# Optimization experiments

Measured on AMD Instinct MI355X. Metric: run time of the kernel, lower is better.

## Reference

```python
import jax, jax.numpy as jnp
import numpy as np

B, D, F, FH = 8, 16, 16, 128
L = D * D
EPS = 1e-5


def _coords():
    i = np.arange(L, dtype=np.float64)
    c0 = ((i + 1) / D - D / 2) / (D / 2)
    c1 = ((i + 1) % D - D / 2) / (D / 2)
    return jnp.asarray(np.stack([c0, c1], axis=1), dtype=jnp.float32)  # (L, 2)


def setup_inputs() -> dict:
    key = jax.random.key(0)
    ks = jax.random.split(key, 16)
    s = 0.05
    fin = F + 2
    inp = {
        "x": jax.random.normal(ks[0], (B, F, D, D), jnp.float32),
        # g_fc1 weight split into the x_i half (first f+2 cols) and x_j half
        "W1a": jax.random.normal(ks[1], (fin, FH), jnp.float32) * s,
        "W1b": jax.random.normal(ks[2], (fin, FH), jnp.float32) * s,
        "b1": jnp.zeros((FH,), jnp.float32),
        "g1_gamma": jnp.ones((FH,), jnp.float32), "g1_beta": jnp.zeros((FH,), jnp.float32),
        "W2": jax.random.normal(ks[3], (FH, FH), jnp.float32) * s, "b2": jnp.zeros((FH,), jnp.float32),
        "g2_gamma": jnp.ones((FH,), jnp.float32), "g2_beta": jnp.zeros((FH,), jnp.float32),
        "W3": jax.random.normal(ks[4], (FH, FH), jnp.float32) * s, "b3": jnp.zeros((FH,), jnp.float32),
        "g3_gamma": jnp.ones((FH,), jnp.float32), "g3_beta": jnp.zeros((FH,), jnp.float32),
        "Wagg": jax.random.normal(ks[5], (L,), jnp.float32) * s, "bagg": jnp.zeros((), jnp.float32),
        "Wf": jax.random.normal(ks[6], (FH, FH), jnp.float32) * s, "bf": jnp.zeros((FH,), jnp.float32),
        "f_gamma": jnp.ones((FH,), jnp.float32), "f_beta": jnp.zeros((FH,), jnp.float32),
        "Wo2": jax.random.normal(ks[7], (FH, FH), jnp.float32) * s, "bo2": jnp.zeros((FH,), jnp.float32),
        "o2_gamma": jnp.ones((FH,), jnp.float32), "o2_beta": jnp.zeros((FH,), jnp.float32),
        "Wo3": jax.random.normal(ks[8], (FH, F), jnp.float32) * s, "bo3": jnp.zeros((F,), jnp.float32),
        "coord": _coords(),
    }
    return inp


def _bn(h, gamma, beta):
    # torch BatchNorm1d (training mode) applied over channel dim = last axis here;
    # stats over (batch, length), biased variance.
    mu = jnp.mean(h, axis=(0, 1))
    var = jnp.mean((h - mu) ** 2, axis=(0, 1))
    return gamma * (h - mu) * jax.lax.rsqrt(var + EPS) + beta


def reference(x, W1a, W1b, b1, g1_gamma, g1_beta, W2, b2, g2_gamma, g2_beta,
              W3, b3, g3_gamma, g3_beta, Wagg, bagg, Wf, bf, f_gamma, f_beta,
              Wo2, bo2, o2_gamma, o2_beta, Wo3, bo3, coord):
    b, f, d = x.shape[0], x.shape[1], x.shape[2]
    l = d * d
    x_flat = x.reshape(b, f, l).transpose(0, 2, 1)                     # (b, L, f)
    x_flat = jnp.concatenate([x_flat, jnp.broadcast_to(coord, (b, l, 2))], axis=2)  # (b, L, f+2)
    # g_fc1 on cat([x_i, x_j]): x_i varies along pair-dim2 (index l), x_j along dim1 (index k)
    hi = x_flat @ W1a                                                  # (b, L, FH)
    hj = x_flat @ W1b                                                  # (b, L, FH)
    h = hi[:, None, :, :] + hj[:, :, None, :] + b1                     # (b, L, L, FH)
    h = h.reshape(b, l * l, -1)
    h = jax.nn.relu(_bn(h, g1_gamma, g1_beta))
    h = jax.nn.relu(_bn(h @ W2 + b2, g2_gamma, g2_beta))
    h = jax.nn.relu(_bn(h @ W3 + b3, g3_gamma, g3_beta))
    x_g = h.reshape(b, l, l, -1)                                       # (b, k, l, FH)
    # affine_aggregate: Linear(L -> 1) over the l (dim2) axis after permute
    x_agg = jnp.einsum('bklf,l->bkf', x_g, Wagg) + bagg                # (b, L, FH)
    x_f = jax.nn.relu(_bn(x_agg @ Wf + bf, f_gamma, f_beta))
    xo = jax.nn.relu(_bn(x_f @ Wo2 + bo2, o2_gamma, o2_beta))
    out = xo @ Wo3 + bo3                                               # (b, L, f)
    return out.reshape(b, d, d, f).transpose(0, 3, 1, 2)               # (b, f, d, d)
```

## Files before the change

### kernel.cpp

```cpp
#include <hip/hip_runtime.h>
#include <hip/hip_bf16.h>

typedef __bf16 bf16x8 __attribute__((ext_vector_type(8)));
typedef float  f32x4  __attribute__((ext_vector_type(4)));

static constexpr size_t HI_OFF  = 0;
static constexpr size_t HJ_OFF  = HI_OFF + (1u << 20);
static constexpr size_t Z_OFF   = HJ_OFF + (1u << 20);
static constexpr size_t PS_OFF  = Z_OFF + (size_t)524288 * 128 * 2;
static constexpr size_t PQ_OFF  = PS_OFF + (size_t)4096 * 128 * 4;
static constexpr size_t S1I_OFF = PQ_OFF + (size_t)4096 * 128 * 4;
static constexpr size_t S2I_OFF = S1I_OFF + 4096;
static constexpr size_t S1J_OFF = S2I_OFF + 4096;
static constexpr size_t S2J_OFF = S1J_OFF + 4096;
static constexpr size_t A1_OFF  = S2J_OFF + 4096;
static constexpr size_t D1_OFF  = A1_OFF + 512;
static constexpr size_t A2_OFF  = D1_OFF + 512;
static constexpr size_t C2_OFF  = A2_OFF + 512;
static constexpr size_t A3_OFF  = C2_OFF + 512;
static constexpr size_t C3_OFF  = A3_OFF + 512;
static constexpr size_t AF_OFF  = C3_OFF + 512;
static constexpr size_t CF_OFF  = AF_OFF + 512;
static constexpr size_t AO_OFF  = CF_OFF + 512;
static constexpr size_t CO_OFF  = AO_OFF + 512;
static constexpr size_t W2T_OFF = CO_OFF + 512;
static constexpr size_t W3T_OFF = W2T_OFF + 32768;
static constexpr size_t XAGG_OFF = W3T_OFF + 32768;
static constexpr size_t Y1_OFF  = XAGG_OFF + (1u << 20);
static constexpr size_t Y2_OFF  = Y1_OFF + (1u << 20);
static constexpr size_t TPS_OFF = Y2_OFF + (1u << 20);
static constexpr size_t TPQ_OFF = TPS_OFF + 65536;

__global__ void build_h(const float* __restrict__ x, const float* __restrict__ coord,
                        const float* __restrict__ W1a, const float* __restrict__ W1b,
                        float* __restrict__ hi, float* __restrict__ hj)
{
    __shared__ float xr[18];
    int bl = blockIdx.x;
    int b = bl >> 8, l = bl & 255;
    int t = threadIdx.x;
    if (t < 18)
        xr[t] = (t < 16) ? x[((size_t)b * 16 + t) * 256 + l] : coord[l * 2 + (t - 16)];
    __syncthreads();
    float ai = 0.f, aj = 0.f;
#pragma unroll
    for (int c = 0; c < 18; ++c) {
        float xv = xr[c];
        ai += xv * W1a[c * 128 + t];
        aj += xv * W1b[c * 128 + t];
    }
    hi[(size_t)bl * 128 + t] = ai;
    hj[(size_t)bl * 128 + t] = aj;
}

__global__ void stats1(const float* __restrict__ hi, const float* __restrict__ hj,
                       float* __restrict__ S1i, float* __restrict__ S2i,
                       float* __restrict__ S1j, float* __restrict__ S2j)
{
    int b = blockIdx.x, f = threadIdx.x;
    float s1i = 0, s2i = 0, s1j = 0, s2j = 0;
    for (int l = 0; l < 256; ++l) {
        float vi = hi[((size_t)b * 256 + l) * 128 + f];
        float vj = hj[((size_t)b * 256 + l) * 128 + f];
        s1i += vi; s2i += vi * vi;
        s1j += vj; s2j += vj * vj;
    }
    S1i[b * 128 + f] = s1i; S2i[b * 128 + f] = s2i;
    S1j[b * 128 + f] = s1j; S2j[b * 128 + f] = s2j;
}

__global__ void bn1_finalize(const float* __restrict__ S1i, const float* __restrict__ S2i,
                             const float* __restrict__ S1j, const float* __restrict__ S2j,
                             const float* __restrict__ g, const float* __restrict__ be,
                             float* __restrict__ a1, float* __restrict__ d1,
                             const float* __restrict__ W2, const float* __restrict__ W3,
                             __bf16* __restrict__ W2t, __bf16* __restrict__ W3t)
{
    int f = threadIdx.x;
    float s1i = 0, s2i = 0, s1j = 0, s2j = 0;
    float mib[8], mjb[8];
#pragma unroll
    for (int b = 0; b < 8; ++b) {
        float x1 = S1i[b * 128 + f]; s1i += x1; mib[b] = x1 * (1.f / 256.f);
        s2i += S2i[b * 128 + f];
        float x2 = S1j[b * 128 + f]; s1j += x2; mjb[b] = x2 * (1.f / 256.f);
        s2j += S2j[b * 128 + f];
    }
    const float invN = 1.f / 2048.f;
    float mi = s1i * invN, mj = s1j * invN;
    float vu = s2i * invN - mi * mi;
    float vv = s2j * invN - mj * mj;
    float cr = 0.f;
#pragma unroll
    for (int b = 0; b < 8; ++b) cr += (mib[b] - mi) * (mjb[b] - mj);
    cr *= (1.f / 8.f);
    float var = vu + vv + 2.f * cr;
    float av = g[f] * rsqrtf(var + 1e-5f);
    a1[f] = av;
    d1[f] = be[f] - av * (mi + mj);
    for (int k = 0; k < 128; ++k) {
        W2t[f * 128 + k] = (__bf16)W2[k * 128 + f];
        W3t[f * 128 + k] = (__bf16)W3[k * 128 + f];
    }
}

__global__ __launch_bounds__(256) void pair_gemm1(
    const float* __restrict__ hi, const float* __restrict__ hj,
    const float* __restrict__ a1, const float* __restrict__ d1,
    const __bf16* __restrict__ W2t,
    __bf16* __restrict__ Z, float* __restrict__ ps, float* __restrict__ pq)
{
    __shared__ __align__(16) char hA[32768];
    __shared__ __align__(16) char wB[32768];
    __shared__ float red[1024];

    int blk = blockIdx.x;
    int half = blk & 1;
    int bk = blk >> 1;
    int b = bk >> 8;
    int t = threadIdx.x;
    int lane = t & 63;
    int wave = t >> 6;
    int fc = (t & 15) * 8;
    int rg = t >> 4;

    float a1v[8], qv[8];
    const float* hjrow = hj + (size_t)bk * 128 + fc;
    const float* d1p = d1 + fc;
    const float* a1p = a1 + fc;
#pragma unroll
    for (int j = 0; j < 8; ++j) { a1v[j] = a1p[j]; qv[j] = a1v[j] * hjrow[j] + d1p[j]; }

    const float* hib = hi + ((size_t)b * 256 + half * 128) * 128;
#pragma unroll
    for (int rr = 0; rr < 128; rr += 16) {
        int row = rr + rg;
        const float* src = hib + row * 128 + fc;
        bf16x8 v;
#pragma unroll
        for (int j = 0; j < 8; ++j) {
            float h = fmaxf(a1v[j] * src[j] + qv[j], 0.f);
            v[j] = (__bf16)h;
        }
        int byte = (row * 256 + fc * 2) ^ ((row & 7) << 4);
        *reinterpret_cast<bf16x8*>(hA + byte) = v;
        bf16x8 w = *reinterpret_cast<const bf16x8*>(W2t + row * 128 + fc);
        *reinterpret_cast<bf16x8*>(wB + byte) = w;
    }
    __syncthreads();

    f32x4 acc[2][8] = {};
    int arow0 = wave * 32 + (lane & 15);
    int kg = (lane >> 4) * 8;
#pragma unroll
    for (int kk = 0; kk < 128; kk += 32) {
        bf16x8 af[2], bfr[8];
#pragma unroll
        for (int m = 0; m < 2; ++m) {
            int row = arow0 + m * 16;
            int byte = (row * 256 + (kk + kg) * 2) ^ ((row & 7) << 4);
            af[m] = *reinterpret_cast<const bf16x8*>(hA + byte);
        }
#pragma unroll
        for (int n = 0; n < 8; ++n) {
            int col = n * 16 + (lane & 15);
            int byte = (col * 256 + (kk + kg) * 2) ^ ((col & 7) << 4);
            bfr[n] = *reinterpret_cast<const bf16x8*>(wB + byte);
        }
#pragma unroll
        for (int m = 0; m < 2; ++m)
#pragma unroll
            for (int n = 0; n < 8; ++n)
                acc[m][n] = __builtin_amdgcn_mfma_f32_16x16x32_bf16(af[m], bfr[n], acc[m][n], 0, 0, 0);
    }

    __bf16* zb = Z + ((size_t)bk * 256 + half * 128) * 128;
    float s[8] = {}, q[8] = {};
    int r0 = (lane >> 4) * 4;
    int cl = lane & 15;
#pragma unroll
    for (int m = 0; m < 2; ++m)
#pragma unroll
        for (int n = 0; n < 8; ++n)
#pragma unroll
            for (int r = 0; r < 4; ++r) {
                float v = acc[m][n][r];
                int row = wave * 32 + m * 16 + r0 + r;
                zb[row * 128 + n * 16 + cl] = (__bf16)v;
                s[n] += v; q[n] += v * v;
            }
#pragma unroll
    for (int n = 0; n < 8; ++n) {
        s[n] += __shfl_xor(s[n], 16); s[n] += __shfl_xor(s[n], 32);
        q[n] += __shfl_xor(q[n], 16); q[n] += __shfl_xor(q[n], 32);
    }
    if (lane < 16) {
#pragma unroll
        for (int n = 0; n < 8; ++n) {
            red[wave * 256 + n * 16 + cl] = s[n];
            red[wave * 256 + 128 + n * 16 + cl] = q[n];
        }
    }
    __syncthreads();
    {
        int f = t & 127, which = t >> 7;
        float a = red[0 * 256 + which * 128 + f] + red[1 * 256 + which * 128 + f]
                + red[2 * 256 + which * 128 + f] + red[3 * 256 + which * 128 + f];
        if (which == 0) ps[(size_t)blk * 128 + f] = a;
        else            pq[(size_t)blk * 128 + f] = a;
    }
}

__global__ __launch_bounds__(256) void pair_gemm2(
    __bf16* __restrict__ Z,
    const float* __restrict__ a2, const float* __restrict__ c2,
    const __bf16* __restrict__ W3t,
    float* __restrict__ ps, float* __restrict__ pq)
{
    __shared__ __align__(16) char hA[32768];
    __shared__ __align__(16) char wB[32768];
    __shared__ float red[1024];

    int blk = blockIdx.x;
    int half = blk & 1;
    int bk = blk >> 1;
    int t = threadIdx.x;
    int lane = t & 63;
    int wave = t >> 6;
    int fc = (t & 15) * 8;
    int rg = t >> 4;

    float a2v[8], c2v[8];
#pragma unroll
    for (int j = 0; j < 8; ++j) { a2v[j] = a2[fc + j]; c2v[j] = c2[fc + j]; }

    __bf16* zbase = Z + ((size_t)bk * 256 + half * 128) * 128;
#pragma unroll
    for (int rr = 0; rr < 128; rr += 16) {
        int row = rr + rg;
        bf16x8 zv = *reinterpret_cast<const bf16x8*>(zbase + row * 128 + fc);
        bf16x8 v;
#pragma unroll
        for (int j = 0; j < 8; ++j) {
            float h = fmaxf(a2v[j] * (float)zv[j] + c2v[j], 0.f);
            v[j] = (__bf16)h;
        }
        int byte = (row * 256 + fc * 2) ^ ((row & 7) << 4);
        *reinterpret_cast<bf16x8*>(hA + byte) = v;
        bf16x8 w = *reinterpret_cast<const bf16x8*>(W3t + row * 128 + fc);
        *reinterpret_cast<bf16x8*>(wB + byte) = w;
    }
    __syncthreads();

    f32x4 acc[2][8] = {};
    int arow0 = wave * 32 + (lane & 15);
    int kg = (lane >> 4) * 8;
#pragma unroll
    for (int kk = 0; kk < 128; kk += 32) {
        bf16x8 af[2], bfr[8];
#pragma unroll
        for (int m = 0; m < 2; ++m) {
            int row = arow0 + m * 16;
            int byte = (row * 256 + (kk + kg) * 2) ^ ((row & 7) << 4);
            af[m] = *reinterpret_cast<const bf16x8*>(hA + byte);
        }
#pragma unroll
        for (int n = 0; n < 8; ++n) {
            int col = n * 16 + (lane & 15);
            int byte = (col * 256 + (kk + kg) * 2) ^ ((col & 7) << 4);
            bfr[n] = *reinterpret_cast<const bf16x8*>(wB + byte);
        }
#pragma unroll
        for (int m = 0; m < 2; ++m)
#pragma unroll
            for (int n = 0; n < 8; ++n)
                acc[m][n] = __builtin_amdgcn_mfma_f32_16x16x32_bf16(af[m], bfr[n], acc[m][n], 0, 0, 0);
    }

    float s[8] = {}, q[8] = {};
    int r0 = (lane >> 4) * 4;
    int cl = lane & 15;
#pragma unroll
    for (int m = 0; m < 2; ++m)
#pragma unroll
        for (int n = 0; n < 8; ++n)
#pragma unroll
            for (int r = 0; r < 4; ++r) {
                float v = acc[m][n][r];
                int row = wave * 32 + m * 16 + r0 + r;
                zbase[row * 128 + n * 16 + cl] = (__bf16)v;
                s[n] += v; q[n] += v * v;
            }
#pragma unroll
    for (int n = 0; n < 8; ++n) {
        s[n] += __shfl_xor(s[n], 16); s[n] += __shfl_xor(s[n], 32);
        q[n] += __shfl_xor(q[n], 16); q[n] += __shfl_xor(q[n], 32);
    }
    if (lane < 16) {
#pragma unroll
        for (int n = 0; n < 8; ++n) {
            red[wave * 256 + n * 16 + cl] = s[n];
            red[wave * 256 + 128 + n * 16 + cl] = q[n];
        }
    }
    __syncthreads();
    {
        int f = t & 127, which = t >> 7;
        float a = red[0 * 256 + which * 128 + f] + red[1 * 256 + which * 128 + f]
                + red[2 * 256 + which * 128 + f] + red[3 * 256 + which * 128 + f];
        if (which == 0) ps[(size_t)blk * 128 + f] = a;
        else            pq[(size_t)blk * 128 + f] = a;
    }
}

__global__ void finalize_bn(const float* __restrict__ ps, const float* __restrict__ pq,
                            int nblk, float inv_count,
                            const float* __restrict__ gamma, const float* __restrict__ beta,
                            float* __restrict__ a, float* __restrict__ c)
{
    __shared__ float rs[256], rq[256];
    int f = blockIdx.x, t = threadIdx.x;
    float s = 0, q = 0;
    for (int i = t; i < nblk; i += 256) {
        s += ps[(size_t)i * 128 + f];
        q += pq[(size_t)i * 128 + f];
    }
    rs[t] = s; rq[t] = q;
    __syncthreads();
    for (int st = 128; st > 0; st >>= 1) {
        if (t < st) { rs[t] += rs[t + st]; rq[t] += rq[t + st]; }
        __syncthreads();
    }
    if (t == 0) {
        float mean = rs[0] * inv_count;
        float var = rq[0] * inv_count - mean * mean;
        float av = gamma[f] * rsqrtf(var + 1e-5f);
        a[f] = av;
        c[f] = beta[f] - av * mean;
    }
}

__global__ void aggregate(const __bf16* __restrict__ Z,
                          const float* __restrict__ a3, const float* __restrict__ c3,
                          const float* __restrict__ Wagg, const float* __restrict__ bagg,
                          float* __restrict__ xagg)
{
    int bk = blockIdx.x;
    int f = threadIdx.x;
    const __bf16* zb = Z + (size_t)bk * 256 * 128 + f;
    float av = a3[f], cv = c3[f];
    float acc = 0.f;
#pragma unroll 4
    for (int l = 0; l < 256; ++l) {
        float v = (float)zb[(size_t)l * 128];
        v = fmaxf(av * v + cv, 0.f);
        acc += v * Wagg[l];
    }
    xagg[(size_t)bk * 128 + f] = acc + bagg[0];
}

__global__ void tail_gemm(const float* __restrict__ X,
                          const float* __restrict__ aIn, const float* __restrict__ cIn, int relu_in,
                          const float* __restrict__ W, const float* __restrict__ bias,
                          float* __restrict__ Y, float* __restrict__ ps, float* __restrict__ pq)
{
    __shared__ float xs[2048];
    __shared__ float rsum[256];
    int blk = blockIdx.x, t = threadIdx.x;
    for (int i = t; i < 2048; i += 256) {
        float v = X[(size_t)blk * 2048 + i];
        if (relu_in) { int f = i & 127; v = fmaxf(aIn[f] * v + cIn[f], 0.f); }
        xs[i] = v;
    }
    __syncthreads();
    int col = t & 127, hf = t >> 7;
    float bv = bias[col];
    float acc[8];
#pragma unroll
    for (int r = 0; r < 8; ++r) acc[r] = bv;
    for (int k = 0; k < 128; ++k) {
        float w = W[k * 128 + col];
#pragma unroll
        for (int r = 0; r < 8; ++r) acc[r] += xs[(hf * 8 + r) * 128 + k] * w;
    }
    float s = 0, q = 0;
#pragma unroll
    for (int r = 0; r < 8; ++r) {
        Y[((size_t)blk * 16 + hf * 8 + r) * 128 + col] = acc[r];
        s += acc[r]; q += acc[r] * acc[r];
    }
    rsum[t] = s; __syncthreads();
    if (hf == 0) ps[(size_t)blk * 128 + col] = rsum[col] + rsum[128 + col];
    __syncthreads();
    rsum[t] = q; __syncthreads();
    if (hf == 0) pq[(size_t)blk * 128 + col] = rsum[col] + rsum[128 + col];
}

__global__ void tail_out(const float* __restrict__ Y2,
                         const float* __restrict__ ao, const float* __restrict__ co,
                         const float* __restrict__ Wo3, const float* __restrict__ bo3,
                         float* __restrict__ out)
{
    __shared__ float xs[2048];
    int blk = blockIdx.x, t = threadIdx.x;
    for (int i = t; i < 2048; i += 256) {
        int f = i & 127;
        xs[i] = fmaxf(ao[f] * Y2[(size_t)blk * 2048 + i] + co[f], 0.f);
    }
    __syncthreads();
    int col = t & 15, r = t >> 4;
    float acc = bo3[col];
    for (int k = 0; k < 128; ++k) acc += xs[r * 128 + k] * Wo3[k * 16 + col];
    int grow = blk * 16 + r;
    int b = grow >> 8, l = grow & 255;
    out[((size_t)b * 16 + col) * 256 + l] = acc;
}

extern "C" void kernel_launch(void* const* d_in, const int* in_sizes, int n_in,
                              void* d_out, int out_size, void* d_ws, size_t ws_size,
                              hipStream_t stream)
{
    const float* x     = (const float*)d_in[0];
    const float* W1a   = (const float*)d_in[1];
    const float* W1b   = (const float*)d_in[2];
    const float* g1g   = (const float*)d_in[4];
    const float* g1b   = (const float*)d_in[5];
    const float* W2    = (const float*)d_in[6];
    const float* g2g   = (const float*)d_in[8];
    const float* g2b   = (const float*)d_in[9];
    const float* W3    = (const float*)d_in[10];
    const float* g3g   = (const float*)d_in[12];
    const float* g3b   = (const float*)d_in[13];
    const float* Wagg  = (const float*)d_in[14];
    const float* bagg  = (const float*)d_in[15];
    const float* Wf    = (const float*)d_in[16];
    const float* bf_   = (const float*)d_in[17];
    const float* fg    = (const float*)d_in[18];
    const float* fb    = (const float*)d_in[19];
    const float* Wo2   = (const float*)d_in[20];
    const float* bo2   = (const float*)d_in[21];
    const float* og    = (const float*)d_in[22];
    const float* ob    = (const float*)d_in[23];
    const float* Wo3   = (const float*)d_in[24];
    const float* bo3   = (const float*)d_in[25];
    const float* coord = (const float*)d_in[26];

    char* ws = (char*)d_ws;
    float*  HI   = (float*)(ws + HI_OFF);
    float*  HJ   = (float*)(ws + HJ_OFF);
    __bf16* Z    = (__bf16*)(ws + Z_OFF);
    float*  PS   = (float*)(ws + PS_OFF);
    float*  PQ   = (float*)(ws + PQ_OFF);
    float*  S1I  = (float*)(ws + S1I_OFF);
    float*  S2I  = (float*)(ws + S2I_OFF);
    float*  S1J  = (float*)(ws + S1J_OFF);
    float*  S2J  = (float*)(ws + S2J_OFF);
    float*  A1   = (float*)(ws + A1_OFF);
    float*  D1   = (float*)(ws + D1_OFF);
    float*  A2   = (float*)(ws + A2_OFF);
    float*  C2   = (float*)(ws + C2_OFF);
    float*  A3   = (float*)(ws + A3_OFF);
    float*  C3   = (float*)(ws + C3_OFF);
    float*  AF   = (float*)(ws + AF_OFF);
    float*  CF   = (float*)(ws + CF_OFF);
    float*  AO   = (float*)(ws + AO_OFF);
    float*  CO   = (float*)(ws + CO_OFF);
    __bf16* W2T  = (__bf16*)(ws + W2T_OFF);
    __bf16* W3T  = (__bf16*)(ws + W3T_OFF);
    float*  XAGG = (float*)(ws + XAGG_OFF);
    float*  Y1   = (float*)(ws + Y1_OFF);
    float*  Y2   = (float*)(ws + Y2_OFF);
    float*  TPS  = (float*)(ws + TPS_OFF);
    float*  TPQ  = (float*)(ws + TPQ_OFF);

    build_h<<<2048, 128, 0, stream>>>(x, coord, W1a, W1b, HI, HJ);
    stats1<<<8, 128, 0, stream>>>(HI, HJ, S1I, S2I, S1J, S2J);
    bn1_finalize<<<1, 128, 0, stream>>>(S1I, S2I, S1J, S2J, g1g, g1b, A1, D1, W2, W3, W2T, W3T);

    pair_gemm1<<<4096, 256, 0, stream>>>(HI, HJ, A1, D1, W2T, Z, PS, PQ);
    finalize_bn<<<128, 256, 0, stream>>>(PS, PQ, 4096, 1.f / 524288.f, g2g, g2b, A2, C2);

    pair_gemm2<<<4096, 256, 0, stream>>>(Z, A2, C2, W3T, PS, PQ);
    finalize_bn<<<128, 256, 0, stream>>>(PS, PQ, 4096, 1.f / 524288.f, g3g, g3b, A3, C3);

    aggregate<<<2048, 128, 0, stream>>>(Z, A3, C3, Wagg, bagg, XAGG);

    tail_gemm<<<128, 256, 0, stream>>>(XAGG, A1, D1, 0, Wf, bf_, Y1, TPS, TPQ);
    finalize_bn<<<128, 256, 0, stream>>>(TPS, TPQ, 128, 1.f / 2048.f, fg, fb, AF, CF);

    tail_gemm<<<128, 256, 0, stream>>>(Y1, AF, CF, 1, Wo2, bo2, Y2, TPS, TPQ);
    finalize_bn<<<128, 256, 0, stream>>>(TPS, TPQ, 128, 1.f / 2048.f, og, ob, AO, CO);

    tail_out<<<128, 256, 0, stream>>>(Y2, AO, CO, Wo3, bo3, (float*)d_out);

    (void)in_sizes; (void)n_in; (void)out_size; (void)ws_size;
}
```

Baseline: 217.1 us.

## Shrink pair GEMM tiles, hold weights in registers, vectorize aggregate

Each pair GEMM block now covers 64 rows instead of 128, doubling the grid to 8192 blocks. Each wave keeps its 32-column slice of the weight matrix in registers, loaded straight from global memory, so the shared-memory weight tile and the cross-wave stats reduction go away and LDS per block drops to 16KB. Each wave writes its own column partial sums directly, so the partial-stat buffers double in size. The aggregate kernel now reads bf16x8 vectors from 16 row groups and reduces them through shared memory instead of making strided scalar loads. The aims are higher occupancy, coalesced loads and less LDS traffic, at the cost of more blocks and more partial-sum work in the finalize step.

```diff
diff --git a/kernel.cpp b/kernel.cpp
--- a/kernel.cpp
+++ b/kernel.cpp
@@ -8,8 +8,8 @@
 static constexpr size_t HJ_OFF  = HI_OFF + (1u << 20);
 static constexpr size_t Z_OFF   = HJ_OFF + (1u << 20);
 static constexpr size_t PS_OFF  = Z_OFF + (size_t)524288 * 128 * 2;
-static constexpr size_t PQ_OFF  = PS_OFF + (size_t)4096 * 128 * 4;
-static constexpr size_t S1I_OFF = PQ_OFF + (size_t)4096 * 128 * 4;
+static constexpr size_t PQ_OFF  = PS_OFF + (size_t)8192 * 128 * 4;
+static constexpr size_t S1I_OFF = PQ_OFF + (size_t)8192 * 128 * 4;
 static constexpr size_t S2I_OFF = S1I_OFF + 4096;
 static constexpr size_t S1J_OFF = S2I_OFF + 4096;
 static constexpr size_t S2J_OFF = S1J_OFF + 4096;
@@ -104,212 +104,196 @@
     }
 }
 
-__global__ __launch_bounds__(256) void pair_gemm1(
+__global__ __launch_bounds__(256, 4) void pair_gemm1(
     const float* __restrict__ hi, const float* __restrict__ hj,
     const float* __restrict__ a1, const float* __restrict__ d1,
     const __bf16* __restrict__ W2t,
     __bf16* __restrict__ Z, float* __restrict__ ps, float* __restrict__ pq)
 {
-    __shared__ __align__(16) char hA[32768];
-    __shared__ __align__(16) char wB[32768];
-    __shared__ float red[1024];
+    __shared__ __align__(16) char hA[16384];
 
     int blk = blockIdx.x;
-    int half = blk & 1;
-    int bk = blk >> 1;
-    int b = bk >> 8;
+    int q   = blk & 3;
+    int bk  = blk >> 2;
+    int b   = bk >> 8;
     int t = threadIdx.x;
     int lane = t & 63;
     int wave = t >> 6;
-    int fc = (t & 15) * 8;
-    int rg = t >> 4;
+    int fc = t & 15;
+    int rbase = t >> 4;
 
     float a1v[8], qv[8];
-    const float* hjrow = hj + (size_t)bk * 128 + fc;
-    const float* d1p = d1 + fc;
-    const float* a1p = a1 + fc;
-#pragma unroll
-    for (int j = 0; j < 8; ++j) { a1v[j] = a1p[j]; qv[j] = a1v[j] * hjrow[j] + d1p[j]; }
-
-    const float* hib = hi + ((size_t)b * 256 + half * 128) * 128;
-#pragma unroll
-    for (int rr = 0; rr < 128; rr += 16) {
-        int row = rr + rg;
-        const float* src = hib + row * 128 + fc;
+    {
+        const float* a1p = a1 + fc * 8;
+        const float* d1p = d1 + fc * 8;
+        const float* hjp = hj + (size_t)bk * 128 + fc * 8;
+#pragma unroll
+        for (int j = 0; j < 8; ++j) { a1v[j] = a1p[j]; qv[j] = a1v[j] * hjp[j] + d1p[j]; }
+    }
+
+    const float* hib = hi + ((size_t)b * 256 + q * 64) * 128;
+#pragma unroll
+    for (int i = 0; i < 4; ++i) {
+        int row = rbase + 16 * i;
+        const float* src = hib + row * 128 + fc * 8;
+        f32x4 u0 = *reinterpret_cast<const f32x4*>(src);
+        f32x4 u1 = *reinterpret_cast<const f32x4*>(src + 4);
         bf16x8 v;
 #pragma unroll
-        for (int j = 0; j < 8; ++j) {
-            float h = fmaxf(a1v[j] * src[j] + qv[j], 0.f);
-            v[j] = (__bf16)h;
+        for (int j = 0; j < 4; ++j) {
+            v[j]     = (__bf16)fmaxf(a1v[j] * u0[j] + qv[j], 0.f);
+            v[j + 4] = (__bf16)fmaxf(a1v[j + 4] * u1[j] + qv[j + 4], 0.f);
         }
-        int byte = (row * 256 + fc * 2) ^ ((row & 7) << 4);
+        int byte = row * 256 + ((fc * 16) ^ ((row & 7) << 4));
         *reinterpret_cast<bf16x8*>(hA + byte) = v;
-        bf16x8 w = *reinterpret_cast<const bf16x8*>(W2t + row * 128 + fc);
-        *reinterpret_cast<bf16x8*>(wB + byte) = w;
-    }
-    __syncthreads();
-
-    f32x4 acc[2][8] = {};
-    int arow0 = wave * 32 + (lane & 15);
-    int kg = (lane >> 4) * 8;
-#pragma unroll
-    for (int kk = 0; kk < 128; kk += 32) {
-        bf16x8 af[2], bfr[8];
-#pragma unroll
-        for (int m = 0; m < 2; ++m) {
-            int row = arow0 + m * 16;
-            int byte = (row * 256 + (kk + kg) * 2) ^ ((row & 7) << 4);
-            af[m] = *reinterpret_cast<const bf16x8*>(hA + byte);
+    }
+
+    int cl = lane & 15, kg = lane >> 4;
+    bf16x8 Bf[2][4];
+#pragma unroll
+    for (int n = 0; n < 2; ++n) {
+        const __bf16* wp = W2t + (wave * 32 + n * 16 + cl) * 128 + kg * 8;
+#pragma unroll
+        for (int kk = 0; kk < 4; ++kk)
+            Bf[n][kk] = *reinterpret_cast<const bf16x8*>(wp + kk * 32);
+    }
+    __syncthreads();
+
+    f32x4 acc[4][2] = {};
+#pragma unroll
+    for (int kk = 0; kk < 4; ++kk) {
+        int kbyte = (kk * 32 + kg * 8) * 2;
+        bf16x8 Af[4];
+#pragma unroll
+        for (int m = 0; m < 4; ++m) {
+            int row = m * 16 + cl;
+            int byte = row * 256 + (kbyte ^ ((row & 7) << 4));
+            Af[m] = *reinterpret_cast<const bf16x8*>(hA + byte);
         }
 #pragma unroll
-        for (int n = 0; n < 8; ++n) {
-            int col = n * 16 + (lane & 15);
-            int byte = (col * 256 + (kk + kg) * 2) ^ ((col & 7) << 4);
-            bfr[n] = *reinterpret_cast<const bf16x8*>(wB + byte);
-        }
-#pragma unroll
-        for (int m = 0; m < 2; ++m)
-#pragma unroll
-            for (int n = 0; n < 8; ++n)
-                acc[m][n] = __builtin_amdgcn_mfma_f32_16x16x32_bf16(af[m], bfr[n], acc[m][n], 0, 0, 0);
-    }
-
-    __bf16* zb = Z + ((size_t)bk * 256 + half * 128) * 128;
-    float s[8] = {}, q[8] = {};
-    int r0 = (lane >> 4) * 4;
-    int cl = lane & 15;
-#pragma unroll
-    for (int m = 0; m < 2; ++m)
-#pragma unroll
-        for (int n = 0; n < 8; ++n)
+        for (int m = 0; m < 4; ++m)
+#pragma unroll
+            for (int n = 0; n < 2; ++n)
+                acc[m][n] = __builtin_amdgcn_mfma_f32_16x16x32_bf16(Af[m], Bf[n][kk], acc[m][n], 0, 0, 0);
+    }
+
+    __bf16* zb = Z + ((size_t)bk * 256 + q * 64) * 128;
+    float s[2] = {}, qq[2] = {};
+#pragma unroll
+    for (int m = 0; m < 4; ++m)
+#pragma unroll
+        for (int n = 0; n < 2; ++n)
 #pragma unroll
             for (int r = 0; r < 4; ++r) {
                 float v = acc[m][n][r];
-                int row = wave * 32 + m * 16 + r0 + r;
-                zb[row * 128 + n * 16 + cl] = (__bf16)v;
-                s[n] += v; q[n] += v * v;
+                int row = m * 16 + kg * 4 + r;
+                int col = wave * 32 + n * 16 + cl;
+                zb[row * 128 + col] = (__bf16)v;
+                s[n] += v; qq[n] += v * v;
             }
 #pragma unroll
-    for (int n = 0; n < 8; ++n) {
+    for (int n = 0; n < 2; ++n) {
         s[n] += __shfl_xor(s[n], 16); s[n] += __shfl_xor(s[n], 32);
-        q[n] += __shfl_xor(q[n], 16); q[n] += __shfl_xor(q[n], 32);
+        qq[n] += __shfl_xor(qq[n], 16); qq[n] += __shfl_xor(qq[n], 32);
     }
     if (lane < 16) {
 #pragma unroll
-        for (int n = 0; n < 8; ++n) {
-            red[wave * 256 + n * 16 + cl] = s[n];
-            red[wave * 256 + 128 + n * 16 + cl] = q[n];
+        for (int n = 0; n < 2; ++n) {
+            int col = wave * 32 + n * 16 + cl;
+            ps[(size_t)blk * 128 + col] = s[n];
+            pq[(size_t)blk * 128 + col] = qq[n];
         }
     }
-    __syncthreads();
-    {
-        int f = t & 127, which = t >> 7;
-        float a = red[0 * 256 + which * 128 + f] + red[1 * 256 + which * 128 + f]
-                + red[2 * 256 + which * 128 + f] + red[3 * 256 + which * 128 + f];
-        if (which == 0) ps[(size_t)blk * 128 + f] = a;
-        else            pq[(size_t)blk * 128 + f] = a;
-    }
-}
-
-__global__ __launch_bounds__(256) void pair_gemm2(
+}
+
+__global__ __launch_bounds__(256, 4) void pair_gemm2(
     __bf16* __restrict__ Z,
     const float* __restrict__ a2, const float* __restrict__ c2,
     const __bf16* __restrict__ W3t,
     float* __restrict__ ps, float* __restrict__ pq)
 {
-    __shared__ __align__(16) char hA[32768];
-    __shared__ __align__(16) char wB[32768];
-    __shared__ float red[1024];
+    __shared__ __align__(16) char hA[16384];
 
     int blk = blockIdx.x;
-    int half = blk & 1;
-    int bk = blk >> 1;
+    int q   = blk & 3;
+    int bk  = blk >> 2;
     int t = threadIdx.x;
     int lane = t & 63;
     int wave = t >> 6;
-    int fc = (t & 15) * 8;
-    int rg = t >> 4;
+    int fc = t & 15;
+    int rbase = t >> 4;
 
     float a2v[8], c2v[8];
 #pragma unroll
-    for (int j = 0; j < 8; ++j) { a2v[j] = a2[fc + j]; c2v[j] = c2[fc + j]; }
-
-    __bf16* zbase = Z + ((size_t)bk * 256 + half * 128) * 128;
-#pragma unroll
-    for (int rr = 0; rr < 128; rr += 16) {
-        int row = rr + rg;
-        bf16x8 zv = *reinterpret_cast<const bf16x8*>(zbase + row * 128 + fc);
+    for (int j = 0; j < 8; ++j) { a2v[j] = a2[fc * 8 + j]; c2v[j] = c2[fc * 8 + j]; }
+
+    __bf16* zbase = Z + ((size_t)bk * 256 + q * 64) * 128;
+#pragma unroll
+    for (int i = 0; i < 4; ++i) {
+        int row = rbase + 16 * i;
+        bf16x8 zv = *reinterpret_cast<const bf16x8*>(zbase + row * 128 + fc * 8);
         bf16x8 v;
 #pragma unroll
-        for (int j = 0; j < 8; ++j) {
-            float h = fmaxf(a2v[j] * (float)zv[j] + c2v[j], 0.f);
-            v[j] = (__bf16)h;
+        for (int j = 0; j < 8; ++j)
+            v[j] = (__bf16)fmaxf(a2v[j] * (float)zv[j] + c2v[j], 0.f);
+        int byte = row * 256 + ((fc * 16) ^ ((row & 7) << 4));
+        *reinterpret_cast<bf16x8*>(hA + byte) = v;
+    }
+
+    int cl = lane & 15, kg = lane >> 4;
+    bf16x8 Bf[2][4];
+#pragma unroll
+    for (int n = 0; n < 2; ++n) {
+        const __bf16* wp = W3t + (wave * 32 + n * 16 + cl) * 128 + kg * 8;
+#pragma unroll
+        for (int kk = 0; kk < 4; ++kk)
+            Bf[n][kk] = *reinterpret_cast<const bf16x8*>(wp + kk * 32);
+    }
+    __syncthreads();
+
+    f32x4 acc[4][2] = {};
+#pragma unroll
+    for (int kk = 0; kk < 4; ++kk) {
+        int kbyte = (kk * 32 + kg * 8) * 2;
+        bf16x8 Af[4];
+#pragma unroll
+        for (int m = 0; m < 4; ++m) {
+            int row = m * 16 + cl;
+            int byte = row * 256 + (kbyte ^ ((row & 7) << 4));
+            Af[m] = *reinterpret_cast<const bf16x8*>(hA + byte);
         }
-        int byte = (row * 256 + fc * 2) ^ ((row & 7) << 4);
-        *reinterpret_cast<bf16x8*>(hA + byte) = v;
-        bf16x8 w = *reinterpret_cast<const bf16x8*>(W3t + row * 128 + fc);
-        *reinterpret_cast<bf16x8*>(wB + byte) = w;
-    }
-    __syncthreads();
-
-    f32x4 acc[2][8] = {};
-    int arow0 = wave * 32 + (lane & 15);
-    int kg = (lane >> 4) * 8;
-#pragma unroll
-    for (int kk = 0; kk < 128; kk += 32) {
-        bf16x8 af[2], bfr[8];
-#pragma unroll
-        for (int m = 0; m < 2; ++m) {
-            int row = arow0 + m * 16;
-            int byte = (row * 256 + (kk + kg) * 2) ^ ((row & 7) << 4);
-            af[m] = *reinterpret_cast<const bf16x8*>(hA + byte);
-        }
-#pragma unroll
-        for (int n = 0; n < 8; ++n) {
-            int col = n * 16 + (lane & 15);
-            int byte = (col * 256 + (kk + kg) * 2) ^ ((col & 7) << 4);
-            bfr[n] = *reinterpret_cast<const bf16x8*>(wB + byte);
-        }
-#pragma unroll
-        for (int m = 0; m < 2; ++m)
-#pragma unroll
-            for (int n = 0; n < 8; ++n)
-                acc[m][n] = __builtin_amdgcn_mfma_f32_16x16x32_bf16(af[m], bfr[n], acc[m][n], 0, 0, 0);
-    }
-
-    float s[8] = {}, q[8] = {};
-    int r0 = (lane >> 4) * 4;
-    int cl = lane & 15;
-#pragma unroll
-    for (int m = 0; m < 2; ++m)
-#pragma unroll
-        for (int n = 0; n < 8; ++n)
+#pragma unroll
+        for (int m = 0; m < 4; ++m)
+#pragma unroll
+            for (int n = 0; n < 2; ++n)
+                acc[m][n] = __builtin_amdgcn_mfma_f32_16x16x32_bf16(Af[m], Bf[n][kk], acc[m][n], 0, 0, 0);
+    }
+
+    float s[2] = {}, qq[2] = {};
+#pragma unroll
+    for (int m = 0; m < 4; ++m)
+#pragma unroll
+        for (int n = 0; n < 2; ++n)
 #pragma unroll
             for (int r = 0; r < 4; ++r) {
                 float v = acc[m][n][r];
-                int row = wave * 32 + m * 16 + r0 + r;
-                zbase[row * 128 + n * 16 + cl] = (__bf16)v;
-                s[n] += v; q[n] += v * v;
+                int row = m * 16 + kg * 4 + r;
+                int col = wave * 32 + n * 16 + cl;
+                zbase[row * 128 + col] = (__bf16)v;
+                s[n] += v; qq[n] += v * v;
             }
 #pragma unroll
-    for (int n = 0; n < 8; ++n) {
+    for (int n = 0; n < 2; ++n) {
         s[n] += __shfl_xor(s[n], 16); s[n] += __shfl_xor(s[n], 32);
-        q[n] += __shfl_xor(q[n], 16); q[n] += __shfl_xor(q[n], 32);
+        qq[n] += __shfl_xor(qq[n], 16); qq[n] += __shfl_xor(qq[n], 32);
     }
     if (lane < 16) {
 #pragma unroll
-        for (int n = 0; n < 8; ++n) {
-            red[wave * 256 + n * 16 + cl] = s[n];
-            red[wave * 256 + 128 + n * 16 + cl] = q[n];
+        for (int n = 0; n < 2; ++n) {
+            int col = wave * 32 + n * 16 + cl;
+            ps[(size_t)blk * 128 + col] = s[n];
+            pq[(size_t)blk * 128 + col] = qq[n];
         }
-    }
-    __syncthreads();
-    {
-        int f = t & 127, which = t >> 7;
-        float a = red[0 * 256 + which * 128 + f] + red[1 * 256 + which * 128 + f]
-                + red[2 * 256 + which * 128 + f] + red[3 * 256 + which * 128 + f];
-        if (which == 0) ps[(size_t)blk * 128 + f] = a;
-        else            pq[(size_t)blk * 128 + f] = a;
     }
 }
 
@@ -340,23 +324,41 @@
     }
 }
 
-__global__ void aggregate(const __bf16* __restrict__ Z,
-                          const float* __restrict__ a3, const float* __restrict__ c3,
-                          const float* __restrict__ Wagg, const float* __restrict__ bagg,
-                          float* __restrict__ xagg)
-{
+__global__ __launch_bounds__(256) void aggregate(
+    const __bf16* __restrict__ Z,
+    const float* __restrict__ a3, const float* __restrict__ c3,
+    const float* __restrict__ Wagg, const float* __restrict__ bagg,
+    float* __restrict__ xagg)
+{
+    __shared__ float red[16 * 128];
     int bk = blockIdx.x;
-    int f = threadIdx.x;
-    const __bf16* zb = Z + (size_t)bk * 256 * 128 + f;
-    float av = a3[f], cv = c3[f];
-    float acc = 0.f;
+    int t = threadIdx.x;
+    int fc = t & 15;
+    int g = t >> 4;
+    float av[8], cv[8];
+#pragma unroll
+    for (int j = 0; j < 8; ++j) { av[j] = a3[fc * 8 + j]; cv[j] = c3[fc * 8 + j]; }
+
+    const __bf16* zb = Z + (size_t)bk * 256 * 128;
+    float acc[8] = {};
 #pragma unroll 4
-    for (int l = 0; l < 256; ++l) {
-        float v = (float)zb[(size_t)l * 128];
-        v = fmaxf(av * v + cv, 0.f);
-        acc += v * Wagg[l];
-    }
-    xagg[(size_t)bk * 128 + f] = acc + bagg[0];
+    for (int i = 0; i < 16; ++i) {
+        int l = g * 16 + i;
+        bf16x8 zv = *reinterpret_cast<const bf16x8*>(zb + (size_t)l * 128 + fc * 8);
+        float w = Wagg[l];
+#pragma unroll
+        for (int j = 0; j < 8; ++j)
+            acc[j] += fmaxf(av[j] * (float)zv[j] + cv[j], 0.f) * w;
+    }
+#pragma unroll
+    for (int j = 0; j < 8; ++j) red[g * 128 + fc * 8 + j] = acc[j];
+    __syncthreads();
+    if (t < 128) {
+        float s = 0;
+#pragma unroll
+        for (int gg = 0; gg < 16; ++gg) s += red[gg * 128 + t];
+        xagg[(size_t)bk * 128 + t] = s + bagg[0];
+    }
 }
 
 __global__ void tail_gemm(const float* __restrict__ X,
@@ -477,13 +479,13 @@
     stats1<<<8, 128, 0, stream>>>(HI, HJ, S1I, S2I, S1J, S2J);
     bn1_finalize<<<1, 128, 0, stream>>>(S1I, S2I, S1J, S2J, g1g, g1b, A1, D1, W2, W3, W2T, W3T);
 
-    pair_gemm1<<<4096, 256, 0, stream>>>(HI, HJ, A1, D1, W2T, Z, PS, PQ);
-    finalize_bn<<<128, 256, 0, stream>>>(PS, PQ, 4096, 1.f / 524288.f, g2g, g2b, A2, C2);
-
-    pair_gemm2<<<4096, 256, 0, stream>>>(Z, A2, C2, W3T, PS, PQ);
-    finalize_bn<<<128, 256, 0, stream>>>(PS, PQ, 4096, 1.f / 524288.f, g3g, g3b, A3, C3);
-
-    aggregate<<<2048, 128, 0, stream>>>(Z, A3, C3, Wagg, bagg, XAGG);
+    pair_gemm1<<<8192, 256, 0, stream>>>(HI, HJ, A1, D1, W2T, Z, PS, PQ);
+    finalize_bn<<<128, 256, 0, stream>>>(PS, PQ, 8192, 1.f / 524288.f, g2g, g2b, A2, C2);
+
+    pair_gemm2<<<8192, 256, 0, stream>>>(Z, A2, C2, W3T, PS, PQ);
+    finalize_bn<<<128, 256, 0, stream>>>(PS, PQ, 8192, 1.f / 524288.f, g3g, g3b, A3, C3);
+
+    aggregate<<<2048, 256, 0, stream>>>(Z, A3, C3, Wagg, bagg, XAGG);
 
     tail_gemm<<<128, 256, 0, stream>>>(XAGG, A1, D1, 0, Wf, bf_, Y1, TPS, TPQ);
     finalize_bn<<<128, 256, 0, stream>>>(TPS, TPQ, 128, 1.f / 2048.f, fg, fb, AF, CF);
```

Result: slower. 253.1 us (+16.6%).
